# Kernel optimization log

Measured on AMD Instinct MI355X. Metric: run time of the kernel, lower is better.

The kernel has to match this reference:

```python
import jax, jax.numpy as jnp
import numpy as np

HIDDEN = 512
STATE_DIM = 256
H = 8
D = STATE_DIM // H  # 32
B = 8
T = 4096


def setup_inputs() -> dict:
    key = jax.random.key(0)
    ks = jax.random.split(key, 12)
    s = 0.02
    return {
        "hidden_states": jax.random.normal(ks[0], (B, T, HIDDEN), jnp.float32),
        "state": jnp.zeros((B, H, D, D), jnp.float32),
        "W_k": jax.random.normal(ks[1], (STATE_DIM, HIDDEN), jnp.float32) * s,
        "W_v": jax.random.normal(ks[2], (STATE_DIM, HIDDEN), jnp.float32) * s,
        "W_q": jax.random.normal(ks[3], (STATE_DIM, HIDDEN), jnp.float32) * s,
        "W_beta": jax.random.normal(ks[4], (STATE_DIM, HIDDEN), jnp.float32) * s,
        "b_beta": jnp.zeros((STATE_DIM,), jnp.float32),
        "W_alpha": jax.random.normal(ks[5], (STATE_DIM, HIDDEN), jnp.float32) * s,
        "b_alpha": jnp.full((STATE_DIM,), 2.0, jnp.float32),
        "W_out": jax.random.normal(ks[6], (HIDDEN, STATE_DIM), jnp.float32) * s,
        "gate_W": jax.random.normal(ks[7], (STATE_DIM, HIDDEN), jnp.float32) * s,
        "norm_w": jnp.ones((STATE_DIM,), jnp.float32),
    }


def _rms_norm(x, w, eps=1e-6):
    dtype = x.dtype
    xf = x.astype(jnp.float32)
    n = xf * jax.lax.rsqrt(jnp.mean(xf * xf, axis=-1, keepdims=True) + eps)
    return (n * w).astype(dtype)


def reference(hidden_states, state, W_k, W_v, W_q, W_beta, b_beta, W_alpha, b_alpha, W_out, gate_W, norm_w):
    bsz, seq_len, _ = hidden_states.shape
    # projections -> (B, T, H, D)
    k = (hidden_states @ W_k.T).reshape(bsz, seq_len, H, D)
    v = (hidden_states @ W_v.T).reshape(bsz, seq_len, H, D)
    q = (hidden_states @ W_q.T).reshape(bsz, seq_len, H, D)
    beta = jax.nn.sigmoid(hidden_states @ W_beta.T + b_beta).reshape(bsz, seq_len, H, D)
    alpha = jax.nn.sigmoid(hidden_states @ W_alpha.T + b_alpha).reshape(bsz, seq_len, H, D)
    # F.normalize(k, dim=-1) with eps=1e-12
    k = k / jnp.maximum(jnp.linalg.norm(k, axis=-1, keepdims=True), 1e-12)
    gate = hidden_states @ gate_W.T  # (B, T, STATE_DIM)

    # time-major for scan: (T, B, H, D)
    def tm(x):
        return jnp.swapaxes(x, 0, 1)

    def step(S, inp):
        k_t, v_t, q_t, b_t, a_t = inp
        S = S * a_t[..., None]                              # row-wise decay
        pred = jnp.einsum('bhij,bhj->bhi', S, k_t)
        S = S + jnp.einsum('bhi,bhj->bhij', b_t * (v_t - pred), k_t)
        readout = jnp.einsum('bhij,bhj->bhi', S, q_t)       # (B, H, D)
        return S, readout

    S_final, readouts = jax.lax.scan(step, state, (tm(k), tm(v), tm(q), tm(beta), tm(alpha)))
    context = jnp.swapaxes(readouts, 0, 1).reshape(bsz, seq_len, STATE_DIM)
    context = _rms_norm(context, norm_w) * jax.nn.silu(gate)
    output = context @ W_out.T
    return output, S_final
```

## Files before the change

### kernel.cpp

```cpp
#include <hip/hip_runtime.h>
#include <stdint.h>

#define B_    8
#define T_    4096
#define HID   512
#define SD    256
#define NH    8
#define HD    32
#define M_TOK (B_*T_)

typedef __attribute__((ext_vector_type(8))) short short8;
typedef __attribute__((ext_vector_type(4))) float f32x4;
typedef __attribute__((ext_vector_type(4))) float f4;
typedef __attribute__((ext_vector_type(2))) float f2;

__device__ __forceinline__ unsigned short f2bf(float f) {
  uint32_t u = __float_as_uint(f);
  uint32_t r = (u + 0x7fffu + ((u >> 16) & 1u)) >> 16;
  return (unsigned short)r;
}

__device__ __forceinline__ void gload16(const void* g, void* l) {
  __builtin_amdgcn_global_load_lds((const __attribute__((address_space(1))) void*)g,
                                   (__attribute__((address_space(3))) void*)l,
                                   16, 0, 0);
}

__device__ __forceinline__ float qred16(float x) {
  x += __int_as_float(__builtin_amdgcn_mov_dpp(__float_as_int(x), 0xB1,  0xF, 0xF, true));
  x += __int_as_float(__builtin_amdgcn_mov_dpp(__float_as_int(x), 0x4E,  0xF, 0xF, true));
  x += __int_as_float(__builtin_amdgcn_mov_dpp(__float_as_int(x), 0x141, 0xF, 0xF, true));
  x += __int_as_float(__builtin_amdgcn_mov_dpp(__float_as_int(x), 0x128, 0xF, 0xF, true));
  return x;
}

__device__ __forceinline__ float dpp_xor1(float x) {
  return __int_as_float(__builtin_amdgcn_mov_dpp(__float_as_int(x), 0xB1, 0xF, 0xF, true));
}

__global__ void cvt_f32_bf16(const float* __restrict__ in, unsigned short* __restrict__ out, int n4) {
  int i = blockIdx.x * blockDim.x + threadIdx.x;
  int stride = gridDim.x * blockDim.x;
  for (; i < n4; i += stride) {
    float4 v = reinterpret_cast<const float4*>(in)[i];
    ushort4 o;
    o.x = f2bf(v.x); o.y = f2bf(v.y); o.z = f2bf(v.z); o.w = f2bf(v.w);
    reinterpret_cast<ushort4*>(out)[i] = o;
  }
}

__global__ void __launch_bounds__(256) cvt_weights(
    const float* __restrict__ W_k, const float* __restrict__ W_v,
    const float* __restrict__ W_q, const float* __restrict__ W_beta,
    const float* __restrict__ W_alpha, const float* __restrict__ gate_W,
    const float* __restrict__ W_out,
    unsigned short* __restrict__ Wc, unsigned short* __restrict__ Wob)
{
  int slice = blockIdx.y;
  const float* src = (slice == 0) ? W_k : (slice == 1) ? W_v : (slice == 2) ? W_q :
                     (slice == 3) ? W_beta : (slice == 4) ? W_alpha : (slice == 5) ? gate_W : W_out;
  unsigned short* dst = (slice == 6) ? Wob : (Wc + slice * 131072);
  int i = blockIdx.x * 256 + threadIdx.x;
  float4 v = reinterpret_cast<const float4*>(src)[i];
  ushort4 o;
  o.x = f2bf(v.x); o.y = f2bf(v.y); o.z = f2bf(v.z); o.w = f2bf(v.w);
  reinterpret_cast<ushort4*>(dst)[i] = o;
}

#define PM 128
#define PN 64
#define PK 64

__global__ void __launch_bounds__(256) proj_gemm(
    const unsigned short* __restrict__ hb, const unsigned short* __restrict__ Wc,
    const float* __restrict__ b_beta, const float* __restrict__ b_alpha,
    float* __restrict__ KQi, float* __restrict__ AVBf, float* __restrict__ gate)
{
  __shared__ unsigned short Asm[PM*PK];
  __shared__ unsigned short Bsm[3][PN*PK];
  const int t = threadIdx.x;
  const int w = t >> 6, lane = t & 63;
  const int bm0 = blockIdx.x * PM;
  const int role = blockIdx.y;
  const int grp = role >> 2;
  const int bn0 = (role & 3) * 64;
  const int pr0 = grp ? 4 : 0, pr1 = grp ? 1 : 2, pr2 = grp ? 3 : 5;

  f32x4 acc[3][2][4];
  #pragma unroll
  for (int pp = 0; pp < 3; ++pp)
    #pragma unroll
    for (int i = 0; i < 2; ++i)
      #pragma unroll
      for (int j = 0; j < 4; ++j) acc[pp][i][j] = (f32x4){0.f, 0.f, 0.f, 0.f};

  for (int k0 = 0; k0 < HID; k0 += PK) {
    #pragma unroll
    for (int it = 0; it < 4; ++it) {
      int unit = t + it * 256;
      int row = unit >> 3, seg = unit & 7;
      int dseg = seg ^ (row & 7);
      const unsigned short* g = hb + (size_t)(bm0 + row) * HID + k0 + dseg * 8;
      gload16(g, (char*)Asm + (w * 1024 + it * 4096));
    }
    #pragma unroll
    for (int pp = 0; pp < 3; ++pp) {
      const int pr = (pp == 0) ? pr0 : (pp == 1) ? pr1 : pr2;
      #pragma unroll
      for (int it = 0; it < 2; ++it) {
        int unit = t + it * 256;
        int n = unit >> 3, seg = unit & 7;
        int dseg = seg ^ (n & 7);
        const unsigned short* g = Wc + (size_t)(pr * 256 + bn0 + n) * HID + k0 + dseg * 8;
        gload16(g, (char*)Bsm[pp] + (w * 1024 + it * 4096));
      }
    }
    __syncthreads();
    #pragma unroll
    for (int ks = 0; ks < 2; ++ks) {
      short8 af[2];
      int u = ks * 4 + (lane >> 4);
      int slot = u ^ (lane & 7);
      #pragma unroll
      for (int rb = 0; rb < 2; ++rb) {
        int row = w * 32 + rb * 16 + (lane & 15);
        af[rb] = *(const short8*)((const char*)Asm + row * 128 + slot * 16);
      }
      #pragma unroll
      for (int pp = 0; pp < 3; ++pp) {
        short8 bfr[4];
        #pragma unroll
        for (int cb = 0; cb < 4; ++cb) {
          int nn = cb * 16 + (lane & 15);
          bfr[cb] = *(const short8*)((const char*)Bsm[pp] + nn * 128 + slot * 16);
        }
        #pragma unroll
        for (int rb = 0; rb < 2; ++rb)
          #pragma unroll
          for (int cb = 0; cb < 4; ++cb)
            acc[pp][rb][cb] = __builtin_amdgcn_mfma_f32_16x16x32_bf16(af[rb], bfr[cb], acc[pp][rb][cb], 0, 0, 0);
      }
    }
    __syncthreads();
  }

  if (grp == 0) {
    #pragma unroll
    for (int rb = 0; rb < 2; ++rb) {
      #pragma unroll
      for (int r = 0; r < 4; ++r) {
        float s0 = acc[0][rb][0][r] * acc[0][rb][0][r] + acc[0][rb][1][r] * acc[0][rb][1][r];
        float s1 = acc[0][rb][2][r] * acc[0][rb][2][r] + acc[0][rb][3][r] * acc[0][rb][3][r];
        s0 = qred16(s0); s1 = qred16(s1);
        float i0 = 1.0f / fmaxf(sqrtf(s0), 1e-12f);
        float i1 = 1.0f / fmaxf(sqrtf(s1), 1e-12f);
        acc[0][rb][0][r] *= i0; acc[0][rb][1][r] *= i0;
        acc[0][rb][2][r] *= i1; acc[0][rb][3][r] *= i1;
      }
    }
    #pragma unroll
    for (int rb = 0; rb < 2; ++rb) {
      #pragma unroll
      for (int cb = 0; cb < 4; ++cb) {
        int rem = bn0 + cb * 16 + (lane & 15);
        int h = rem >> 5, d = rem & 31;
        #pragma unroll
        for (int r = 0; r < 4; ++r) {
          int m = bm0 + w * 32 + rb * 16 + (lane >> 4) * 4 + r;
          int bb = m >> 12, tt = m & 4095;
          size_t tok = ((size_t)(bb * NH + h) * T_ + tt);
          float kv = acc[0][rb][cb][r], qv = acc[1][rb][cb][r];
          float kn = dpp_xor1(kv), qn = dpp_xor1(qv);
          if ((lane & 1) == 0)
            *(float4*)&KQi[tok * 64 + (d >> 1) * 4] = (float4){kv, kn, qv, qn};
          gate[(size_t)m * SD + rem] = acc[2][rb][cb][r];
        }
      }
    }
  } else {
    #pragma unroll
    for (int rb = 0; rb < 2; ++rb) {
      #pragma unroll
      for (int cb = 0; cb < 4; ++cb) {
        int rem = bn0 + cb * 16 + (lane & 15);
        int h = rem >> 5, d = rem & 31;
        #pragma unroll
        for (int r = 0; r < 4; ++r) {
          int m = bm0 + w * 32 + rb * 16 + (lane >> 4) * 4 + r;
          int bb = m >> 12, tt = m & 4095;
          size_t tok = ((size_t)(bb * NH + h) * T_ + tt);
          float av = 1.0f / (1.0f + expf(-(acc[0][rb][cb][r] + b_alpha[rem])));
          float vv = acc[1][rb][cb][r];
          float bv = 1.0f / (1.0f + expf(-(acc[2][rb][cb][r] + b_beta[rem])));
          *(float4*)&AVBf[(tok * HD + d) * 4] = (float4){av, vv, bv, 0.0f};
        }
      }
    }
  }
}

#define CH 32
#define NCH (T_/CH)

#define DSR(dst, areg, imm) \
  asm volatile("ds_read_b128 %0, %1 offset:%c2" : "=v"(dst) : "v"(areg), "i"(imm))

#define SHUF2(V,A,B) __builtin_shufflevector(V, V, A, B)

#define BAR asm volatile("s_barrier" ::: "memory")

__global__ void __launch_bounds__(128, 1) scan_kernel(
    const float* __restrict__ KQi, const float4* __restrict__ AVB,
    const float* __restrict__ state_in,
    float* __restrict__ ctx, float* __restrict__ Sfin)
{
  __shared__ __align__(16) char Lds[20480];
  const int blk = blockIdx.x;
  const int bh = blk & 63, rg = blk >> 6;
  const int b = bh >> 3, h = bh & 7;
  const int tid = threadIdx.x;
  const int wid = tid >> 6;
  const int lw = tid & 63;

  const float*  KQg = KQi + (size_t)bh * (T_ * 64);
  const float4* Vg  = AVB + (size_t)bh * (T_ * HD) + rg * 4;

  const uint32_t lds0 = (uint32_t)(uintptr_t)(__attribute__((address_space(3))) char*)&Lds[0];

  if (wid == 1) {
    const int gpp = lw >> 2, gqt = lw & 3;
    f4 gx0, gx1, gx2, gx3, gy0, gy1, gy2, gy3;
    const uint32_t a_gw = lds0 + 16384 + (2 * gpp) * 64 + gqt * 16 + 12;

    auto stageW = [&](int c2, int buf) {
      const float* kqg = KQg + (size_t)c2 * (CH * 64);
      #pragma unroll
      for (int it = 0; it < 8; ++it)
        gload16(kqg + (size_t)(lw + it * 64) * 4, Lds + buf * 8192 + it * 1024);
      const float4* vg = Vg + (size_t)c2 * (CH * HD);
      #pragma unroll
      for (int it = 0; it < 2; ++it) {
        int tc = it * 16 + (lw >> 2), r = lw & 3;
        gload16(vg + (size_t)tc * HD + r, Lds + 16384 + buf * 2048 + it * 1024);
      }
    };

    auto gfetch = [&](int c2) {
      const float* gp = KQg + ((size_t)c2 * CH + 2 * gpp) * 64 + gqt * 16;
      gx0 = *(const f4*)(gp);      gx1 = *(const f4*)(gp + 4);
      gx2 = *(const f4*)(gp + 8);  gx3 = *(const f4*)(gp + 12);
      gy0 = *(const f4*)(gp + 64); gy1 = *(const f4*)(gp + 68);
      gy2 = *(const f4*)(gp + 72); gy3 = *(const f4*)(gp + 76);
    };

    auto gwrite = [&](int buf) {
      f2 g2 = SHUF2(gx0, 0, 1) * SHUF2(gy0, 0, 1);
      g2 = __builtin_elementwise_fma(SHUF2(gx1, 0, 1), SHUF2(gy1, 0, 1), g2);
      g2 = __builtin_elementwise_fma(SHUF2(gx2, 0, 1), SHUF2(gy2, 0, 1), g2);
      g2 = __builtin_elementwise_fma(SHUF2(gx3, 0, 1), SHUF2(gy3, 0, 1), g2);
      float G = g2.x + g2.y;
      G += __int_as_float(__builtin_amdgcn_mov_dpp(__float_as_int(G), 0xB1, 0xF, 0xF, true));
      G += __int_as_float(__builtin_amdgcn_mov_dpp(__float_as_int(G), 0x4E, 0xF, 0xF, true));
      uint32_t aw = a_gw + buf * 2048;
      asm volatile("ds_write_b32 %0, %1" :: "v"(aw), "v"(G));
      asm volatile("s_waitcnt lgkmcnt(0)" ::: "memory");
    };

    gfetch(0);
    stageW(0, 0);
    asm volatile("s_waitcnt vmcnt(0)" ::: "memory");
    gwrite(0);
    BAR;
    #pragma unroll 1
    for (int c = 0; c < NCH; ++c) {
      if (c + 1 < NCH) {
        gfetch(c + 1);
        stageW(c + 1, (c + 1) & 1);
        asm volatile("s_waitcnt vmcnt(0)" ::: "memory");
        gwrite((c + 1) & 1);
      }
      BAR;
    }
    return;
  }

  const int il = lw >> 4;
  const int p  = lw & 15;

  f2 S2;
  {
    const float* sp = state_in + (size_t)bh * 1024 + (rg * 4 + il) * 32 + p * 2;
    S2 = (f2){sp[0], sp[1]};
  }

  const uint32_t a_kq = lds0 + p * 16;
  const uint32_t a_v  = lds0 + 16384 + il * 16;

  float osel = 0.0f;
  float* ctxp = ctx + (size_t)b * T_ * SD + (size_t)p * SD + h * HD + rg * 4 + il;

  f4 kqA, vvA, kqB, vvB, kqC, vvC, kqD, vvD, kqE, vvE, kqF, vvF;

#define R2(X, Y, BUF, J) do { \
    DSR(kq##X, a_kq, (BUF)*8192 + (2*(J))*256); \
    DSR(vv##X, a_v,  (BUF)*2048 + (2*(J))*64); \
    DSR(kq##Y, a_kq, (BUF)*8192 + (2*(J)+1)*256); \
    DSR(vv##Y, a_v,  (BUF)*2048 + (2*(J)+1)*64); \
  } while (0)

#define WKA2(N, X, Y) \
    asm volatile("s_waitcnt lgkmcnt(" #N ")" \
                 : "+v"(kq##X), "+v"(vv##X), "+v"(kq##Y), "+v"(vv##Y))

#define C2(X, Y, T0) do { \
    f2 k0_ = SHUF2(kq##X, 0, 1), q0_ = SHUF2(kq##X, 2, 3); \
    f2 k1_ = SHUF2(kq##Y, 0, 1), q1_ = SHUF2(kq##Y, 2, 3); \
    f4 VA_ = vv##X, VB_ = vv##Y; \
    f2 dA_ = k0_ * S2, dB_ = k1_ * S2; \
    float W0_ = qred16(dA_.x + dA_.y); \
    float W1_ = qred16(dB_.x + dB_.y); \
    float u0_ = fmaf(-(VA_.z * VA_.x), W0_, VA_.z * VA_.y); \
    float bua_ = VB_.z * VB_.x; \
    float c2_ = bua_ * VA_.w; \
    float c1_ = fmaf(-(bua_ * VA_.x), W1_, VB_.z * VB_.y); \
    float u1_ = fmaf(-c2_, u0_, c1_); \
    f2 St_ = __builtin_elementwise_fma((f2){u0_, u0_}, k0_, (f2){VA_.x, VA_.x} * S2); \
    f2 Su_ = __builtin_elementwise_fma((f2){u1_, u1_}, k1_, (f2){VB_.x, VB_.x} * St_); \
    f2 o0_ = q0_ * St_; \
    f2 o1_ = q1_ * Su_; \
    S2 = Su_; \
    float od0_ = qred16(o0_.x + o0_.y); \
    float od1_ = qred16(o1_.x + o1_.y); \
    osel = (p == ((T0) & 15))       ? od0_ : osel; \
    osel = (p == (((T0) + 1) & 15)) ? od1_ : osel; \
    if ((((T0) + 1) & 15) == 15) { *ctxp = osel; ctxp += 16 * SD; } \
  } while (0)

#define CHUNK(BUF) do { \
    R2(A,B,BUF,0); R2(C,D,BUF,1); R2(E,F,BUF,2); \
    WKA2(8,A,B); C2(A,B, 0); R2(A,B,BUF,3); \
    WKA2(8,C,D); C2(C,D, 2); R2(C,D,BUF,4); \
    WKA2(8,E,F); C2(E,F, 4); R2(E,F,BUF,5); \
    WKA2(8,A,B); C2(A,B, 6); R2(A,B,BUF,6); \
    WKA2(8,C,D); C2(C,D, 8); R2(C,D,BUF,7); \
    WKA2(8,E,F); C2(E,F,10); R2(E,F,BUF,8); \
    WKA2(8,A,B); C2(A,B,12); R2(A,B,BUF,9); \
    WKA2(8,C,D); C2(C,D,14); R2(C,D,BUF,10); \
    WKA2(8,E,F); C2(E,F,16); R2(E,F,BUF,11); \
    WKA2(8,A,B); C2(A,B,18); R2(A,B,BUF,12); \
    WKA2(8,C,D); C2(C,D,20); R2(C,D,BUF,13); \
    WKA2(8,E,F); C2(E,F,22); R2(E,F,BUF,14); \
    WKA2(8,A,B); C2(A,B,24); R2(A,B,BUF,15); \
    WKA2(8,C,D); C2(C,D,26); \
    WKA2(4,E,F); C2(E,F,28); \
    WKA2(0,A,B); C2(A,B,30); \
    BAR; \
  } while (0)

  BAR;
  #pragma unroll 1
  for (int cp = 0; cp < NCH / 2; ++cp) {
    CHUNK(0);
    CHUNK(1);
  }

  {
    float* sp = Sfin + (size_t)bh * 1024 + (rg * 4 + il) * 32 + p * 2;
    sp[0] = S2.x; sp[1] = S2.y;
  }
#undef C2
#undef R2
#undef WKA2
#undef CHUNK
}

__global__ void __launch_bounds__(256) rms_silu(
    const float* __restrict__ ctx, const float* __restrict__ gate,
    const float* __restrict__ norm_w, unsigned short* __restrict__ ctx2)
{
  size_t row = (size_t)blockIdx.x * 4 + (threadIdx.x >> 6);
  int lane = threadIdx.x & 63;
  const float4 x = *(const float4*)&ctx[row * SD + lane * 4];
  float s = x.x * x.x + x.y * x.y + x.z * x.z + x.w * x.w;
  #pragma unroll
  for (int m = 32; m >= 1; m >>= 1) s += __shfl_xor(s, m, 64);
  float rs = 1.0f / sqrtf(s * (1.0f / 256.0f) + 1e-6f);
  const float4 g = *(const float4*)&gate[row * SD + lane * 4];
  const float4 w = *(const float4*)&norm_w[lane * 4];
  ushort4 o;
  o.x = f2bf(x.x * rs * w.x * (g.x / (1.0f + expf(-g.x))));
  o.y = f2bf(x.y * rs * w.y * (g.y / (1.0f + expf(-g.y))));
  o.z = f2bf(x.z * rs * w.z * (g.z / (1.0f + expf(-g.z))));
  o.w = f2bf(x.w * rs * w.w * (g.w / (1.0f + expf(-g.w))));
  *(ushort4*)&ctx2[row * SD + lane * 4] = o;
}

__global__ void __launch_bounds__(256) out_gemm(
    const unsigned short* __restrict__ ctx2, const unsigned short* __restrict__ Wob,
    float* __restrict__ out)
{
  __shared__ unsigned short Asm[PM*PK];
  __shared__ unsigned short Bsm[PN*PK];
  const int t = threadIdx.x;
  const int w = t >> 6, lane = t & 63;
  const int bm0 = blockIdx.x * PM;
  const int bn0 = blockIdx.y * PN;

  f32x4 acc[2][4];
  #pragma unroll
  for (int i = 0; i < 2; ++i)
    #pragma unroll
    for (int j = 0; j < 4; ++j) acc[i][j] = (f32x4){0.f, 0.f, 0.f, 0.f};

  for (int k0 = 0; k0 < SD; k0 += PK) {
    #pragma unroll
    for (int it = 0; it < 4; ++it) {
      int unit = t + it * 256;
      int row = unit >> 3, seg = unit & 7;
      int dseg = seg ^ (row & 7);
      const unsigned short* g = ctx2 + (size_t)(bm0 + row) * SD + k0 + dseg * 8;
      gload16(g, (char*)Asm + (w * 1024 + it * 4096));
    }
    #pragma unroll
    for (int it = 0; it < 2; ++it) {
      int unit = t + it * 256;
      int n = unit >> 3, seg = unit & 7;
      int dseg = seg ^ (n & 7);
      const unsigned short* g = Wob + (size_t)(bn0 + n) * SD + k0 + dseg * 8;
      gload16(g, (char*)Bsm + (w * 1024 + it * 4096));
    }
    __syncthreads();
    #pragma unroll
    for (int ks = 0; ks < 2; ++ks) {
      short8 af[2], bfr[4];
      int u = ks * 4 + (lane >> 4);
      int slot = u ^ (lane & 7);
      #pragma unroll
      for (int rb = 0; rb < 2; ++rb) {
        int row = w * 32 + rb * 16 + (lane & 15);
        af[rb] = *(const short8*)((const char*)Asm + row * 128 + slot * 16);
      }
      #pragma unroll
      for (int cb = 0; cb < 4; ++cb) {
        int nn = cb * 16 + (lane & 15);
        bfr[cb] = *(const short8*)((const char*)Bsm + nn * 128 + slot * 16);
      }
      #pragma unroll
      for (int rb = 0; rb < 2; ++rb)
        #pragma unroll
        for (int cb = 0; cb < 4; ++cb)
          acc[rb][cb] = __builtin_amdgcn_mfma_f32_16x16x32_bf16(af[rb], bfr[cb], acc[rb][cb], 0, 0, 0);
    }
    __syncthreads();
  }
  #pragma unroll
  for (int rb = 0; rb < 2; ++rb)
    #pragma unroll
    for (int cb = 0; cb < 4; ++cb) {
      int n = bn0 + cb * 16 + (lane & 15);
      #pragma unroll
      for (int r = 0; r < 4; ++r) {
        int m = bm0 + w * 32 + rb * 16 + (lane >> 4) * 4 + r;
        out[(size_t)m * 512 + n] = acc[rb][cb][r];
      }
    }
}

extern "C" void kernel_launch(void* const* d_in, const int* in_sizes, int n_in,
                              void* d_out, int out_size, void* d_ws, size_t ws_size,
                              hipStream_t stream) {
  (void)in_sizes; (void)n_in; (void)out_size; (void)ws_size;
  const float* hidden  = (const float*)d_in[0];
  const float* state   = (const float*)d_in[1];
  const float* W_k     = (const float*)d_in[2];
  const float* W_v     = (const float*)d_in[3];
  const float* W_q     = (const float*)d_in[4];
  const float* W_beta  = (const float*)d_in[5];
  const float* b_beta  = (const float*)d_in[6];
  const float* W_alpha = (const float*)d_in[7];
  const float* b_alpha = (const float*)d_in[8];
  const float* W_out   = (const float*)d_in[9];
  const float* gate_W  = (const float*)d_in[10];
  const float* norm_w  = (const float*)d_in[11];
  float* out = (float*)d_out;

  char* ws = (char*)d_ws;
  unsigned short* hb  = (unsigned short*)(ws);
  unsigned short* Wc  = (unsigned short*)(ws + 33554432);
  unsigned short* Wob = (unsigned short*)(ws + 35127296);
  float* KQi  = (float*)(ws + 35389440);
  float* AVBf = (float*)(ws + 102498304);
  unsigned short* ctx2 = (unsigned short*)(ws + 236716032);
  float* ctx  = out;
  float* gate = out + 8388608;
  float* Sfin = out + 16777216;

  cvt_f32_bf16<<<2048, 256, 0, stream>>>(hidden, hb, M_TOK * HID / 4);
  cvt_weights<<<dim3(128, 7), 256, 0, stream>>>(W_k, W_v, W_q, W_beta, W_alpha, gate_W, W_out, Wc, Wob);

  proj_gemm<<<dim3(256, 8), 256, 0, stream>>>(hb, Wc, b_beta, b_alpha, KQi, AVBf, gate);
  scan_kernel<<<512, 128, 0, stream>>>(KQi, (const float4*)AVBf, state, ctx, Sfin);
  rms_silu<<<8192, 256, 0, stream>>>(ctx, gate, norm_w, ctx2);
  out_gemm<<<dim3(256, 8), 256, 0, stream>>>(ctx2, Wob, out);
}
```

Measured before the change: 399.3 us.

## Offload scan readout reductions to producer wave via LDS partial sums

The compute wave no longer performs the two 16-lane cross-lane reductions per timestep pair for the readout. It writes per-lane partial dot products to a double-buffered LDS region, and the loader wave reduces them one chunk behind and writes the context output. This takes DPP reduction work off the serial recurrence critical path. In exchange it adds LDS writes, changes the waitcnt accounting and uses more shared memory, while the loader wave does extra work between barriers.

```diff
diff --git a/kernel.cpp b/kernel.cpp
--- a/kernel.cpp
+++ b/kernel.cpp
@@ -205,16 +205,20 @@
 #define DSR(dst, areg, imm) \
   asm volatile("ds_read_b128 %0, %1 offset:%c2" : "=v"(dst) : "v"(areg), "i"(imm))
 
+#define DSW64(areg, val, imm) \
+  asm volatile("ds_write_b64 %0, %1 offset:%c2" :: "v"(areg), "v"(val), "i"(imm))
+
 #define SHUF2(V,A,B) __builtin_shufflevector(V, V, A, B)
 
 #define BAR asm volatile("s_barrier" ::: "memory")
+#define WK0 asm volatile("s_waitcnt lgkmcnt(0)" ::: "memory")
 
 __global__ void __launch_bounds__(128, 1) scan_kernel(
     const float* __restrict__ KQi, const float4* __restrict__ AVB,
     const float* __restrict__ state_in,
     float* __restrict__ ctx, float* __restrict__ Sfin)
 {
-  __shared__ __align__(16) char Lds[20480];
+  __shared__ __align__(16) char Lds[36864];
   const int blk = blockIdx.x;
   const int bh = blk & 63, rg = blk >> 6;
   const int b = bh >> 3, h = bh & 7;
@@ -228,9 +232,11 @@
   const uint32_t lds0 = (uint32_t)(uintptr_t)(__attribute__((address_space(3))) char*)&Lds[0];
 
   if (wid == 1) {
+    const int il1 = lw >> 4, p1 = lw & 15;
     const int gpp = lw >> 2, gqt = lw & 3;
     f4 gx0, gx1, gx2, gx3, gy0, gy1, gy2, gy3;
     const uint32_t a_gw = lds0 + 16384 + (2 * gpp) * 64 + gqt * 16 + 12;
+    float* ctxb = ctx + (size_t)b * T_ * SD + h * HD + rg * 4 + il1;
 
     auto stageW = [&](int c2, int buf) {
       const float* kqg = KQg + (size_t)c2 * (CH * 64);
@@ -266,6 +272,23 @@
       asm volatile("s_waitcnt lgkmcnt(0)" ::: "memory");
     };
 
+    auto reduceC = [&](int cc) {
+      const char* rbase = (const char*)Lds + 20480 + (cc & 1) * 8192;
+      #pragma unroll
+      for (int half = 0; half < 2; ++half) {
+        float osel = 0.0f;
+        #pragma unroll
+        for (int pr = 0; pr < 8; ++pr) {
+          f2 v = *(const f2*)(rbase + (half * 8 + pr) * 512 + lw * 8);
+          float rx = qred16(v.x);
+          float ry = qred16(v.y);
+          osel = (p1 == 2 * pr)     ? rx : osel;
+          osel = (p1 == 2 * pr + 1) ? ry : osel;
+        }
+        ctxb[(size_t)(cc * 32 + half * 16 + p1) * SD] = osel;
+      }
+    };
+
     gfetch(0);
     stageW(0, 0);
     asm volatile("s_waitcnt vmcnt(0)" ::: "memory");
@@ -273,14 +296,15 @@
     BAR;
     #pragma unroll 1
     for (int c = 0; c < NCH; ++c) {
+      if (c + 1 < NCH) { gfetch(c + 1); stageW(c + 1, (c + 1) & 1); }
+      if (c > 0) reduceC(c - 1);
       if (c + 1 < NCH) {
-        gfetch(c + 1);
-        stageW(c + 1, (c + 1) & 1);
         asm volatile("s_waitcnt vmcnt(0)" ::: "memory");
         gwrite((c + 1) & 1);
       }
       BAR;
     }
+    reduceC(NCH - 1);
     return;
   }
 
@@ -295,9 +319,7 @@
 
   const uint32_t a_kq = lds0 + p * 16;
   const uint32_t a_v  = lds0 + 16384 + il * 16;
-
-  float osel = 0.0f;
-  float* ctxp = ctx + (size_t)b * T_ * SD + (size_t)p * SD + h * HD + rg * 4 + il;
+  const uint32_t a_rw = lds0 + 20480 + lw * 8;
 
   f4 kqA, vvA, kqB, vvB, kqC, vvC, kqD, vvD, kqE, vvE, kqF, vvF;
 
@@ -312,7 +334,7 @@
     asm volatile("s_waitcnt lgkmcnt(" #N ")" \
                  : "+v"(kq##X), "+v"(vv##X), "+v"(kq##Y), "+v"(vv##Y))
 
-#define C2(X, Y, T0) do { \
+#define C2(X, Y, J, BUF) do { \
     f2 k0_ = SHUF2(kq##X, 0, 1), q0_ = SHUF2(kq##X, 2, 3); \
     f2 k1_ = SHUF2(kq##Y, 0, 1), q1_ = SHUF2(kq##Y, 2, 3); \
     f4 VA_ = vv##X, VB_ = vv##Y; \
@@ -329,31 +351,29 @@
     f2 o0_ = q0_ * St_; \
     f2 o1_ = q1_ * Su_; \
     S2 = Su_; \
-    float od0_ = qred16(o0_.x + o0_.y); \
-    float od1_ = qred16(o1_.x + o1_.y); \
-    osel = (p == ((T0) & 15))       ? od0_ : osel; \
-    osel = (p == (((T0) + 1) & 15)) ? od1_ : osel; \
-    if ((((T0) + 1) & 15) == 15) { *ctxp = osel; ctxp += 16 * SD; } \
+    f2 po_ = (f2){o0_.x + o0_.y, o1_.x + o1_.y}; \
+    DSW64(a_rw, po_, (BUF)*8192 + (J)*512); \
   } while (0)
 
 #define CHUNK(BUF) do { \
     R2(A,B,BUF,0); R2(C,D,BUF,1); R2(E,F,BUF,2); \
-    WKA2(8,A,B); C2(A,B, 0); R2(A,B,BUF,3); \
-    WKA2(8,C,D); C2(C,D, 2); R2(C,D,BUF,4); \
-    WKA2(8,E,F); C2(E,F, 4); R2(E,F,BUF,5); \
-    WKA2(8,A,B); C2(A,B, 6); R2(A,B,BUF,6); \
-    WKA2(8,C,D); C2(C,D, 8); R2(C,D,BUF,7); \
-    WKA2(8,E,F); C2(E,F,10); R2(E,F,BUF,8); \
-    WKA2(8,A,B); C2(A,B,12); R2(A,B,BUF,9); \
-    WKA2(8,C,D); C2(C,D,14); R2(C,D,BUF,10); \
-    WKA2(8,E,F); C2(E,F,16); R2(E,F,BUF,11); \
-    WKA2(8,A,B); C2(A,B,18); R2(A,B,BUF,12); \
-    WKA2(8,C,D); C2(C,D,20); R2(C,D,BUF,13); \
-    WKA2(8,E,F); C2(E,F,22); R2(E,F,BUF,14); \
-    WKA2(8,A,B); C2(A,B,24); R2(A,B,BUF,15); \
-    WKA2(8,C,D); C2(C,D,26); \
-    WKA2(4,E,F); C2(E,F,28); \
-    WKA2(0,A,B); C2(A,B,30); \
+    WKA2(8 ,A,B); C2(A,B, 0,BUF); R2(A,B,BUF,3); \
+    WKA2(9 ,C,D); C2(C,D, 1,BUF); R2(C,D,BUF,4); \
+    WKA2(10,E,F); C2(E,F, 2,BUF); R2(E,F,BUF,5); \
+    WKA2(10,A,B); C2(A,B, 3,BUF); R2(A,B,BUF,6); \
+    WKA2(10,C,D); C2(C,D, 4,BUF); R2(C,D,BUF,7); \
+    WKA2(10,E,F); C2(E,F, 5,BUF); R2(E,F,BUF,8); \
+    WKA2(10,A,B); C2(A,B, 6,BUF); R2(A,B,BUF,9); \
+    WKA2(10,C,D); C2(C,D, 7,BUF); R2(C,D,BUF,10); \
+    WKA2(10,E,F); C2(E,F, 8,BUF); R2(E,F,BUF,11); \
+    WKA2(10,A,B); C2(A,B, 9,BUF); R2(A,B,BUF,12); \
+    WKA2(10,C,D); C2(C,D,10,BUF); R2(C,D,BUF,13); \
+    WKA2(10,E,F); C2(E,F,11,BUF); R2(E,F,BUF,14); \
+    WKA2(10,A,B); C2(A,B,12,BUF); R2(A,B,BUF,15); \
+    WKA2(10,C,D); C2(C,D,13,BUF); \
+    WKA2(6 ,E,F); C2(E,F,14,BUF); \
+    WKA2(2 ,A,B); C2(A,B,15,BUF); \
+    WK0; \
     BAR; \
   } while (0)
 
```

Measured after the change: 415.3 us. 4.0% more time.
